# Kernel optimization log

Hardware: AMD Instinct MI355X
Metric: run time of the kernel (lower is better)

## Reference

```python
import jax, jax.numpy as jnp
import numpy as np

B = 8192
D_IN = 512
UNITS = 512


def setup_inputs() -> dict:
    key = jax.random.key(0)
    ks = jax.random.split(key, 9)
    sx = 1.0 / np.sqrt(D_IN)
    sh = 1.0 / np.sqrt(UNITS)
    return {
        "input_x": jax.random.normal(ks[0], (B, D_IN), jnp.float32),
        "input_h": jax.random.normal(ks[1], (B, UNITS), jnp.float32),
        "attention_score": jax.random.uniform(ks[2], (B, 1), jnp.float32),
        "Wx_r": jax.random.normal(ks[3], (D_IN, UNITS), jnp.float32) * sx,
        "b_r": jnp.zeros((UNITS,), jnp.float32),
        "Wh_r": jax.random.normal(ks[4], (UNITS, UNITS), jnp.float32) * sh,
        "Wx_u": jax.random.normal(ks[5], (D_IN, UNITS), jnp.float32) * sx,
        "b_u": jnp.zeros((UNITS,), jnp.float32),
        "Wh_u": jax.random.normal(ks[6], (UNITS, UNITS), jnp.float32) * sh,
        "Wx_h": jax.random.normal(ks[7], (D_IN, UNITS), jnp.float32) * sx,
        "b_h": jnp.zeros((UNITS,), jnp.float32),
        "Wh_h": jax.random.normal(ks[8], (UNITS, UNITS), jnp.float32) * sh,
    }


def reference(input_x, input_h, attention_score,
              Wx_r, b_r, Wh_r,
              Wx_u, b_u, Wh_u,
              Wx_h, b_h, Wh_h):
    # reset gate: sigmoid(Dense_b(x) + Dense(h))
    r = jax.nn.sigmoid(input_x @ Wx_r + b_r + input_h @ Wh_r)
    # update gate: sigmoid(Dense_b(x) + Dense(h))
    u = jax.nn.sigmoid(input_x @ Wx_u + b_u + input_h @ Wh_u)
    # candidate: tanh(Dense_b(x) + r * Dense(h))
    cal_h = jnp.tanh(input_x @ Wx_h + b_h + r * (input_h @ Wh_h))
    # attention-modulated update and interpolation
    u_att = attention_score * u
    h = (1.0 - u_att) * input_h + u_att * cal_h
    return h
```

## Files before the change

kernel.cpp:

```cpp
#include <hip/hip_runtime.h>
#include <hip/hip_bf16.h>

typedef __bf16 bf16x8 __attribute__((ext_vector_type(8)));
typedef float f32x4 __attribute__((ext_vector_type(4)));
typedef unsigned short us8 __attribute__((ext_vector_type(8)));

#define MFMA16 __builtin_amdgcn_mfma_f32_16x16x32_bf16

__device__ __forceinline__ unsigned short f2bf(float f) {
    unsigned int u = __float_as_uint(f);
    u += 0x7fffu + ((u >> 16) & 1u);
    return (unsigned short)(u >> 16);
}

__global__ void cvt_all_kernel(const float* __restrict__ x, const float* __restrict__ h,
                               unsigned short* __restrict__ AP,
                               const float* __restrict__ W0, const float* __restrict__ W1,
                               const float* __restrict__ W2, const float* __restrict__ W3,
                               const float* __restrict__ W4, const float* __restrict__ W5,
                               unsigned short* __restrict__ WP) {
    if (blockIdx.x < 4096) {
        int c = blockIdx.x * 256 + threadIdx.x;
        int ih = c >> 19;
        const float* src = ih ? h : x;
        int c2 = c & 524287;
        int mb = c2 >> 10, kb = (c2 >> 6) & 15, lane = c2 & 63;
        int r = lane & 15, ko = lane >> 4;
        const float* p = src + (size_t)(mb * 16 + r) * 512 + kb * 32 + ko * 8;
        float4 v0 = *(const float4*)p;
        float4 v1 = *(const float4*)(p + 4);
        us8 o = { f2bf(v0.x), f2bf(v0.y), f2bf(v0.z), f2bf(v0.w),
                  f2bf(v1.x), f2bf(v1.y), f2bf(v1.z), f2bf(v1.w) };
        *((us8*)AP + ((size_t)(mb * 32 + kb + ih * 16) << 6) + lane) = o;
    } else {
        int c = (blockIdx.x - 4096) * 256 + threadIdx.x;
        int s = c >> 16, c2 = c & 65535;
        int frag = c2 >> 6, lane = c2 & 63;
        int nb = frag >> 5, kbp = frag & 31;
        const float* Wsrc;
        int kb;
        if (kbp < 16) { kb = kbp;      Wsrc = (s == 0) ? W0 : (s == 1) ? W2 : W4; }
        else          { kb = kbp - 16; Wsrc = (s == 0) ? W1 : (s == 1) ? W3 : W5; }
        int cc = lane & 15, ko = lane >> 4;
        int kbase = kb * 32 + ko * 8;
        us8 o;
#pragma unroll
        for (int e = 0; e < 8; ++e)
            o[e] = f2bf(Wsrc[(size_t)(kbase + e) * 512 + nb * 16 + cc]);
        *((us8*)WP + c) = o;
    }
}

__global__ __launch_bounds__(512, 2) void augru_mm(
    const unsigned short* __restrict__ AP_,
    const unsigned short* __restrict__ WP_,
    const float* __restrict__ b_r, const float* __restrict__ b_u, const float* __restrict__ b_h,
    const float* __restrict__ att, const float* __restrict__ h32,
    float* __restrict__ out) {
    const unsigned char* __restrict__ APb = (const unsigned char*)AP_;
    const unsigned char* __restrict__ WPb = (const unsigned char*)WP_;

    const int t0 = threadIdx.x, wv = t0 >> 6, lane = t0 & 63;
    const int laneoff = lane * 16;

    const int bid = blockIdx.x;
    const int Wid = (bid & 7) * 32 + (bid >> 3);
    const int mblk = Wid >> 3, nblk = Wid & 7;
    const int wr = wv >> 1, wc = wv & 1;

    f32x4 accR[4][2] = {}, accU[4][2] = {}, accXH[4][2] = {}, accHH[4][2] = {};

    const unsigned char* __restrict__ pA[4];
    const unsigned char* __restrict__ pB[3][2];
#pragma unroll
    for (int mf = 0; mf < 4; ++mf)
        pA[mf] = APb + ((size_t)((mblk * 16 + wr * 4 + mf) * 32) << 10) + laneoff;
#pragma unroll
    for (int s = 0; s < 3; ++s)
#pragma unroll
        for (int nf = 0; nf < 2; ++nf)
            pB[s][nf] = WPb + (size_t)s * 1048576 +
                        ((size_t)((nblk * 4 + wc * 2 + nf) * 32) << 10) + laneoff;

    bf16x8 aN[4], bN[3][2];
#pragma unroll
    for (int mf = 0; mf < 4; ++mf) aN[mf] = *(const bf16x8*)(pA[mf]);
#pragma unroll
    for (int s = 0; s < 3; ++s)
#pragma unroll
        for (int nf = 0; nf < 2; ++nf) bN[s][nf] = *(const bf16x8*)(pB[s][nf]);

#define ROTATE_LOAD(T1) { \
    _Pragma("unroll") for (int mf = 0; mf < 4; ++mf) \
        aN[mf] = *(const bf16x8*)(pA[mf] + ((size_t)(T1) << 10)); \
    _Pragma("unroll") for (int s = 0; s < 3; ++s) \
      _Pragma("unroll") for (int nf = 0; nf < 2; ++nf) \
        bN[s][nf] = *(const bf16x8*)(pB[s][nf] + ((size_t)(T1) << 10)); }

#define MFMAS(ACCC) { \
    _Pragma("unroll") for (int mf = 0; mf < 4; ++mf) \
      _Pragma("unroll") for (int nf = 0; nf < 2; ++nf) { \
        accR[mf][nf] = MFMA16(aC[mf], bC[0][nf], accR[mf][nf], 0, 0, 0); \
        accU[mf][nf] = MFMA16(aC[mf], bC[1][nf], accU[mf][nf], 0, 0, 0); \
        ACCC[mf][nf] = MFMA16(aC[mf], bC[2][nf], ACCC[mf][nf], 0, 0, 0); } }

#pragma unroll 2
    for (int T = 0; T < 16; ++T) {
        bf16x8 aC[4], bC[3][2];
#pragma unroll
        for (int mf = 0; mf < 4; ++mf) aC[mf] = aN[mf];
#pragma unroll
        for (int s = 0; s < 3; ++s)
#pragma unroll
            for (int nf = 0; nf < 2; ++nf) bC[s][nf] = bN[s][nf];
        ROTATE_LOAD(T + 1)
        MFMAS(accXH)
    }
#pragma unroll 2
    for (int T = 16; T < 31; ++T) {
        bf16x8 aC[4], bC[3][2];
#pragma unroll
        for (int mf = 0; mf < 4; ++mf) aC[mf] = aN[mf];
#pragma unroll
        for (int s = 0; s < 3; ++s)
#pragma unroll
            for (int nf = 0; nf < 2; ++nf) bC[s][nf] = bN[s][nf];
        ROTATE_LOAD(T + 1)
        MFMAS(accHH)
    }
    {
        bf16x8 aC[4], bC[3][2];
#pragma unroll
        for (int mf = 0; mf < 4; ++mf) aC[mf] = aN[mf];
#pragma unroll
        for (int s = 0; s < 3; ++s)
#pragma unroll
            for (int nf = 0; nf < 2; ++nf) bC[s][nf] = bN[s][nf];
        MFMAS(accHH)
    }

    const int lr = lane & 15, lg = lane >> 4;
#pragma unroll
    for (int nf = 0; nf < 2; ++nf) {
        const int col = nblk * 64 + wc * 32 + nf * 16 + lr;
        const float br = b_r[col], bu = b_u[col], bh = b_h[col];
#pragma unroll
        for (int mf = 0; mf < 4; ++mf) {
            const int rowb = mblk * 256 + wr * 64 + mf * 16 + lg * 4;
#pragma unroll
            for (int q = 0; q < 4; ++q) {
                const int row = rowb + q;
                float r = 1.f / (1.f + __expf(-(accR[mf][nf][q] + br)));
                float u = 1.f / (1.f + __expf(-(accU[mf][nf][q] + bu)));
                float ph = accXH[mf][nf][q] + bh + r * accHH[mf][nf][q];
                ph = fminf(fmaxf(ph, -15.f), 15.f);
                float e = __expf(2.f * ph);
                float cal = (e - 1.f) / (e + 1.f);
                float hv = h32[(size_t)row * 512 + col];
                float ua = att[row] * u;
                out[(size_t)row * 512 + col] = fmaf(ua, cal - hv, hv);
            }
        }
    }
#undef ROTATE_LOAD
#undef MFMAS
}

extern "C" void kernel_launch(void* const* d_in, const int* in_sizes, int n_in,
                              void* d_out, int out_size, void* d_ws, size_t ws_size,
                              hipStream_t stream) {
    const float* x    = (const float*)d_in[0];
    const float* h    = (const float*)d_in[1];
    const float* att  = (const float*)d_in[2];
    const float* Wx_r = (const float*)d_in[3];
    const float* b_r  = (const float*)d_in[4];
    const float* Wh_r = (const float*)d_in[5];
    const float* Wx_u = (const float*)d_in[6];
    const float* b_u  = (const float*)d_in[7];
    const float* Wh_u = (const float*)d_in[8];
    const float* Wx_h = (const float*)d_in[9];
    const float* b_h  = (const float*)d_in[10];
    const float* Wh_h = (const float*)d_in[11];
    float* out = (float*)d_out;

    unsigned short* AP = (unsigned short*)d_ws;
    unsigned short* WP = AP + 8388608;

    cvt_all_kernel<<<4864, 256, 0, stream>>>(x, h, AP,
        Wx_r, Wh_r, Wx_u, Wh_u, Wx_h, Wh_h, WP);
    augru_mm<<<256, 512, 0, stream>>>(AP, WP, b_r, b_u, b_h, att, h, out);
}
```

Before: 54.07 us.

## Shrink GEMM tiles to 32x64 per block with more blocks and double-buffered loads

The fused AUGRU GEMM kernel moves from 256 blocks of 512 threads (256x64 tiles, 4x2 fragments per wave) to 2048 blocks of 256 threads (32x64 tiles, 2x1 fragments per wave). Launch bounds now target 6 blocks per CU, and loads use an explicit two-set ping-pong with s_setprio around the MFMA groups. The aim is higher occupancy and fewer registers per wave, so more waves are available to hide global-load latency. In exchange, each wave gets much less operand reuse, which raises global/L2 traffic for the A and W fragments.

```diff
diff --git a/kernel.cpp b/kernel.cpp
--- a/kernel.cpp
+++ b/kernel.cpp
@@ -51,7 +51,7 @@
     }
 }
 
-__global__ __launch_bounds__(512, 2) void augru_mm(
+__global__ __launch_bounds__(256, 6) void augru_mm(
     const unsigned short* __restrict__ AP_,
     const unsigned short* __restrict__ WP_,
     const float* __restrict__ b_r, const float* __restrict__ b_u, const float* __restrict__ b_h,
@@ -64,106 +64,79 @@
     const int laneoff = lane * 16;
 
     const int bid = blockIdx.x;
-    const int Wid = (bid & 7) * 32 + (bid >> 3);
-    const int mblk = Wid >> 3, nblk = Wid & 7;
-    const int wr = wv >> 1, wc = wv & 1;
+    const int Wid = (bid & 7) * 256 + (bid >> 3);
+    const int mblk = Wid >> 3;
+    const int nblk16 = (Wid & 7) * 4 + wv;
 
-    f32x4 accR[4][2] = {}, accU[4][2] = {}, accXH[4][2] = {}, accHH[4][2] = {};
+    f32x4 accR[2] = {}, accU[2] = {}, accXH[2] = {}, accHH[2] = {};
 
-    const unsigned char* __restrict__ pA[4];
-    const unsigned char* __restrict__ pB[3][2];
+    const unsigned char* __restrict__ pAl = APb + laneoff;
+    const unsigned char* __restrict__ pBl = WPb + laneoff;
+    size_t Aoff[2], Boff[3];
 #pragma unroll
-    for (int mf = 0; mf < 4; ++mf)
-        pA[mf] = APb + ((size_t)((mblk * 16 + wr * 4 + mf) * 32) << 10) + laneoff;
+    for (int mf = 0; mf < 2; ++mf)
+        Aoff[mf] = ((size_t)((mblk * 2 + mf) * 32)) << 10;
 #pragma unroll
     for (int s = 0; s < 3; ++s)
+        Boff[s] = (size_t)s * 1048576 + (((size_t)(nblk16 * 32)) << 10);
+
+    bf16x8 a0[2], a1[2], b0[3], b1[3];
+
+#define LOADSET(S, T) { \
+    _Pragma("unroll") for (int mf = 0; mf < 2; ++mf) \
+        a##S[mf] = *(const bf16x8*)(pAl + Aoff[mf] + ((size_t)(T) << 10)); \
+    _Pragma("unroll") for (int s = 0; s < 3; ++s) \
+        b##S[s] = *(const bf16x8*)(pBl + Boff[s] + ((size_t)(T) << 10)); }
+
+#define MFMASET(S, ACCC) { \
+    __builtin_amdgcn_s_setprio(1); \
+    _Pragma("unroll") for (int mf = 0; mf < 2; ++mf) { \
+        accR[mf] = MFMA16(a##S[mf], b##S[0], accR[mf], 0, 0, 0); \
+        accU[mf] = MFMA16(a##S[mf], b##S[1], accU[mf], 0, 0, 0); \
+        ACCC[mf] = MFMA16(a##S[mf], b##S[2], ACCC[mf], 0, 0, 0); } \
+    __builtin_amdgcn_s_setprio(0); }
+
+    LOADSET(0, 0)
 #pragma unroll
-        for (int nf = 0; nf < 2; ++nf)
-            pB[s][nf] = WPb + (size_t)s * 1048576 +
-                        ((size_t)((nblk * 4 + wc * 2 + nf) * 32) << 10) + laneoff;
-
-    bf16x8 aN[4], bN[3][2];
+    for (int T = 0; T < 16; T += 2) {
+        LOADSET(1, T + 1)
+        MFMASET(0, accXH)
+        LOADSET(0, T + 2)
+        MFMASET(1, accXH)
+    }
 #pragma unroll
-    for (int mf = 0; mf < 4; ++mf) aN[mf] = *(const bf16x8*)(pA[mf]);
-#pragma unroll
-    for (int s = 0; s < 3; ++s)
-#pragma unroll
-        for (int nf = 0; nf < 2; ++nf) bN[s][nf] = *(const bf16x8*)(pB[s][nf]);
-
-#define ROTATE_LOAD(T1) { \
-    _Pragma("unroll") for (int mf = 0; mf < 4; ++mf) \
-        aN[mf] = *(const bf16x8*)(pA[mf] + ((size_t)(T1) << 10)); \
-    _Pragma("unroll") for (int s = 0; s < 3; ++s) \
-      _Pragma("unroll") for (int nf = 0; nf < 2; ++nf) \
-        bN[s][nf] = *(const bf16x8*)(pB[s][nf] + ((size_t)(T1) << 10)); }
-
-#define MFMAS(ACCC) { \
-    _Pragma("unroll") for (int mf = 0; mf < 4; ++mf) \
-      _Pragma("unroll") for (int nf = 0; nf < 2; ++nf) { \
-        accR[mf][nf] = MFMA16(aC[mf], bC[0][nf], accR[mf][nf], 0, 0, 0); \
-        accU[mf][nf] = MFMA16(aC[mf], bC[1][nf], accU[mf][nf], 0, 0, 0); \
-        ACCC[mf][nf] = MFMA16(aC[mf], bC[2][nf], ACCC[mf][nf], 0, 0, 0); } }
-
-#pragma unroll 2
-    for (int T = 0; T < 16; ++T) {
-        bf16x8 aC[4], bC[3][2];
-#pragma unroll
-        for (int mf = 0; mf < 4; ++mf) aC[mf] = aN[mf];
-#pragma unroll
-        for (int s = 0; s < 3; ++s)
-#pragma unroll
-            for (int nf = 0; nf < 2; ++nf) bC[s][nf] = bN[s][nf];
-        ROTATE_LOAD(T + 1)
-        MFMAS(accXH)
+    for (int T = 16; T < 30; T += 2) {
+        LOADSET(1, T + 1)
+        MFMASET(0, accHH)
+        LOADSET(0, T + 2)
+        MFMASET(1, accHH)
     }
-#pragma unroll 2
-    for (int T = 16; T < 31; ++T) {
-        bf16x8 aC[4], bC[3][2];
-#pragma unroll
-        for (int mf = 0; mf < 4; ++mf) aC[mf] = aN[mf];
-#pragma unroll
-        for (int s = 0; s < 3; ++s)
-#pragma unroll
-            for (int nf = 0; nf < 2; ++nf) bC[s][nf] = bN[s][nf];
-        ROTATE_LOAD(T + 1)
-        MFMAS(accHH)
-    }
-    {
-        bf16x8 aC[4], bC[3][2];
-#pragma unroll
-        for (int mf = 0; mf < 4; ++mf) aC[mf] = aN[mf];
-#pragma unroll
-        for (int s = 0; s < 3; ++s)
-#pragma unroll
-            for (int nf = 0; nf < 2; ++nf) bC[s][nf] = bN[s][nf];
-        MFMAS(accHH)
-    }
+    LOADSET(1, 31)
+    MFMASET(0, accHH)
+    MFMASET(1, accHH)
 
     const int lr = lane & 15, lg = lane >> 4;
+    const int col = nblk16 * 16 + lr;
+    const float br = b_r[col], bu = b_u[col], bh = b_h[col];
 #pragma unroll
-    for (int nf = 0; nf < 2; ++nf) {
-        const int col = nblk * 64 + wc * 32 + nf * 16 + lr;
-        const float br = b_r[col], bu = b_u[col], bh = b_h[col];
+    for (int mf = 0; mf < 2; ++mf) {
+        const int rowb = mblk * 32 + mf * 16 + lg * 4;
 #pragma unroll
-        for (int mf = 0; mf < 4; ++mf) {
-            const int rowb = mblk * 256 + wr * 64 + mf * 16 + lg * 4;
-#pragma unroll
-            for (int q = 0; q < 4; ++q) {
-                const int row = rowb + q;
-                float r = 1.f / (1.f + __expf(-(accR[mf][nf][q] + br)));
-                float u = 1.f / (1.f + __expf(-(accU[mf][nf][q] + bu)));
-                float ph = accXH[mf][nf][q] + bh + r * accHH[mf][nf][q];
-                ph = fminf(fmaxf(ph, -15.f), 15.f);
-                float e = __expf(2.f * ph);
-                float cal = (e - 1.f) / (e + 1.f);
-                float hv = h32[(size_t)row * 512 + col];
-                float ua = att[row] * u;
-                out[(size_t)row * 512 + col] = fmaf(ua, cal - hv, hv);
-            }
+        for (int q = 0; q < 4; ++q) {
+            const int row = rowb + q;
+            float r = 1.f / (1.f + __expf(-(accR[mf][q] + br)));
+            float u = 1.f / (1.f + __expf(-(accU[mf][q] + bu)));
+            float ph = accXH[mf][q] + bh + r * accHH[mf][q];
+            ph = fminf(fmaxf(ph, -15.f), 15.f);
+            float e = __expf(2.f * ph);
+            float cal = (e - 1.f) / (e + 1.f);
+            float hv = h32[(size_t)row * 512 + col];
+            float ua = att[row] * u;
+            out[(size_t)row * 512 + col] = fmaf(ua, cal - hv, hv);
         }
     }
-#undef ROTATE_LOAD
-#undef MFMAS
+#undef LOADSET
+#undef MFMASET
 }
 
 extern "C" void kernel_launch(void* const* d_in, const int* in_sizes, int n_in,
@@ -188,5 +161,5 @@
 
     cvt_all_kernel<<<4864, 256, 0, stream>>>(x, h, AP,
         Wx_r, Wh_r, Wx_u, Wh_u, Wx_h, Wh_h, WP);
-    augru_mm<<<256, 512, 0, stream>>>(AP, WP, b_r, b_u, b_h, att, h, out);
+    augru_mm<<<2048, 256, 0, stream>>>(AP, WP, b_r, b_u, b_h, att, h, out);
 }
```

Result: slower. 105.7 us (+95.5%).
